# Performance work log

Measured on AMD Instinct MI355X. Metric: run time of the kernel, lower is better.

The kernel has to match this reference:

```python
import jax, jax.numpy as jnp
import numpy as np

N = 50000       # nodes
E = 500000      # edges
F_IN = 64       # input feature dim
F_OUT = 64      # hidden/output dim
K = 3           # diffusion filter order
C = F_IN + F_OUT  # concat dim seen by each DConv


def _xavier(k, shape):
    fan_in, fan_out = shape[-2], shape[-1]
    lim = float(np.sqrt(6.0 / (fan_in + fan_out)))
    return jax.random.uniform(k, shape, jnp.float32, -lim, lim)


def setup_inputs() -> dict:
    key = jax.random.key(0)
    ks = jax.random.split(key, 8)
    X = jax.random.normal(ks[0], (N, F_IN), jnp.float32)
    H = jax.random.normal(ks[1], (N, F_OUT), jnp.float32)
    # ring edges guarantee every node has in-degree >= 1 and out-degree >= 1
    base = jnp.arange(N, dtype=jnp.int32)
    row = jnp.concatenate([base, jax.random.randint(ks[2], (E - N,), 0, N, jnp.int32)])
    col = jnp.concatenate([jnp.roll(base, 1), jax.random.randint(ks[3], (E - N,), 0, N, jnp.int32)])
    edge_index = jnp.stack([row, col])  # [2, E]
    W_z = _xavier(ks[4], (2, K, C, F_OUT))
    W_r = _xavier(ks[5], (2, K, C, F_OUT))
    W_h = _xavier(ks[6], (2, K, C, F_OUT))
    b = jnp.zeros((F_OUT,), jnp.float32)
    return {"X": X, "edge_index": edge_index, "H": H,
            "W_z": W_z, "b_z": b, "W_r": W_r, "b_r": b, "W_h": W_h, "b_h": b}


def _dconv(Xc, row, col, norm_out, norm_in, W, b):
    # PyG propagate: gather source (row) features, scale by edge norm, scatter-add to target (col)
    def prop(x, norm):
        return jax.ops.segment_sum(norm[:, None] * x[row], col, num_segments=N)
    Tx_0 = Xc
    Hout = Xc @ (W[0, 0] + W[1, 0])
    Tx_1_o = prop(Xc, norm_out)
    Tx_1_i = prop(Xc, norm_in)
    Hout = Hout + Tx_1_o @ W[0, 1] + Tx_1_i @ W[1, 1]
    for k in range(2, K):
        Tx_2_o = 2.0 * prop(Tx_1_o, norm_out) - Tx_0
        Tx_2_i = 2.0 * prop(Tx_1_i, norm_in) - Tx_0
        Hout = Hout + Tx_2_o @ W[0, k] + Tx_2_i @ W[1, k]
        # faithful to original: Tx_1 is never reassigned, so Tx_0 stays Xc
        Tx_0, Tx_1_o, Tx_1_i = Xc, Tx_2_o, Tx_2_i
    return Hout + b


def reference(X, edge_index, H, W_z, b_z, W_r, b_r, W_h, b_h):
    row, col = edge_index[0], edge_index[1]
    deg_out = jnp.zeros((N,), jnp.float32).at[row].add(1.0)
    deg_in = jnp.zeros((N,), jnp.float32).at[col].add(1.0)
    norm_out = (1.0 / deg_out)[row]
    norm_in = (1.0 / deg_in)[row]
    XH = jnp.concatenate([X, H], axis=1)
    Z = jax.nn.sigmoid(_dconv(XH, row, col, norm_out, norm_in, W_z, b_z))
    R = jax.nn.sigmoid(_dconv(XH, row, col, norm_out, norm_in, W_r, b_r))
    XHR = jnp.concatenate([X, H * R], axis=1)
    H_tilde = jnp.tanh(_dconv(XHR, row, col, norm_out, norm_in, W_h, b_h))
    H_new = Z * H + (1.0 - Z) * H_tilde
    # NaN infill with mean of non-NaN entries (faithful to original)
    mask = jnp.isnan(H_new)
    H_new = jnp.where(mask, jnp.nanmean(H_new), H_new)
    return H_new
```

## Files before the change

kernel.cpp:

```cpp
#include <hip/hip_runtime.h>
#include <hip/hip_bf16.h>
#include <math.h>

#define N_NODES 50000
#define N_EDGES 500000
#define C_DIM 128

typedef __attribute__((ext_vector_type(8))) short bf8;
typedef __attribute__((ext_vector_type(4))) float f32x4;

__device__ __forceinline__ float bflo(unsigned u) { return __uint_as_float(u << 16); }
__device__ __forceinline__ float bfhi(unsigned u) { return __uint_as_float(u & 0xffff0000u); }
__device__ __forceinline__ unsigned short f2bfu(float f) {
    __hip_bfloat16 h = __float2bfloat16(f);
    unsigned short u;
    __builtin_memcpy(&u, &h, 2);
    return u;
}
__device__ __forceinline__ unsigned packbf(float a, float b) {
    return ((unsigned)f2bfu(b) << 16) | f2bfu(a);
}


__global__ void count_deg(const int* __restrict__ row, const int* __restrict__ col,
                          int* __restrict__ dout, int* __restrict__ din, int e) {
    int i = blockIdx.x * blockDim.x + threadIdx.x;
    if (i >= e) return;
    atomicAdd(&dout[row[i]], 1);
    atomicAdd(&din[col[i]], 1);
}

__global__ void scan_block(const int* __restrict__ counts, int* __restrict__ excl,
                           int* __restrict__ blocksums, int n) {
    __shared__ int tmp[1024];
    int tid = threadIdx.x;
    int gid = blockIdx.x * 1024 + tid;
    int v = (gid < n) ? counts[gid] : 0;
    tmp[tid] = v;
    __syncthreads();
    for (int off = 1; off < 1024; off <<= 1) {
        int t = (tid >= off) ? tmp[tid - off] : 0;
        __syncthreads();
        tmp[tid] += t;
        __syncthreads();
    }
    int incl = tmp[tid];
    if (gid < n) excl[gid] = incl - v;
    if (tid == 1023) blocksums[blockIdx.x] = incl;
}

__global__ void scan_sums(int* __restrict__ blocksums, int nb) {
    __shared__ int tmp[64];
    int tid = threadIdx.x;
    int v = (tid < nb) ? blocksums[tid] : 0;
    tmp[tid] = v;
    __syncthreads();
    for (int off = 1; off < 64; off <<= 1) {
        int t = (tid >= off) ? tmp[tid - off] : 0;
        __syncthreads();
        tmp[tid] += t;
        __syncthreads();
    }
    if (tid < nb) blocksums[tid] = tmp[tid] - v;
}

__global__ void scan_add(int* __restrict__ rowptr, const int* __restrict__ blocksums,
                         int* __restrict__ cursor, const int* __restrict__ dout,
                         const int* __restrict__ din, float2* __restrict__ winv,
                         int n, int e_total) {
    int gid = blockIdx.x * blockDim.x + threadIdx.x;
    if (gid < n) {
        int v = rowptr[gid] + blocksums[gid >> 10];
        rowptr[gid] = v;
        cursor[gid] = v;
        winv[gid] = make_float2(1.0f / (float)dout[gid], 1.0f / (float)din[gid]);
    }
    if (gid == n) rowptr[n] = e_total;
}

__global__ void build_csr(const int* __restrict__ row, const int* __restrict__ col,
                          const float2* __restrict__ winv,
                          int* __restrict__ cursor, int* __restrict__ src,
                          float2* __restrict__ w, int e) {
    int i = blockIdx.x * blockDim.x + threadIdx.x;
    if (i >= e) return;
    int r = row[i], c = col[i];
    int pos = atomicAdd(&cursor[c], 1);
    src[pos] = r;
    w[pos] = winv[r];
}

__device__ __forceinline__ float wraw(const float* W, int d, int kk, int k, int j) {
    return W[((d * 3 + kk) * 128 + k) * 64 + j];
}

__global__ void pack_weights(const float* __restrict__ Wz, const float* __restrict__ Wr,
                             const float* __restrict__ Wh,
                             unsigned short* __restrict__ Wzr_t,
                             unsigned short* __restrict__ Wh_t) {
    int i = blockIdx.x * blockDim.x + threadIdx.x;
    if (i < 128 * 640) {
        int k = i % 640;
        int nn = i / 640;
        const float* W = (nn < 64) ? Wz : Wr;
        int j = nn & 63;
        float v;
        if (k < 128) {
            v = wraw(W, 0, 0, k, j) + wraw(W, 1, 0, k, j);
        } else {
            int k2 = k - 128;
            int kk = (k2 >= 256) ? 2 : 1;
            int k3 = k2 & 255;
            int p = k3 >> 2, sub = k3 & 3;
            v = wraw(W, sub >> 1, kk, 2 * p + (sub & 1), j);
        }
        Wzr_t[i] = f2bfu(v);
    } else if (i < 128 * 640 + 64 * 640) {
        int i2 = i - 128 * 640;
        int k = i2 % 640;
        int j = i2 / 640;
        float v;
        if (k < 64) {
            v = wraw(Wh, 0, 0, k, j) + wraw(Wh, 1, 0, k, j);
        } else if (k < 320) {
            int k2 = k - 64;
            int kk = (k2 >= 128) ? 2 : 1;
            int k3 = k2 & 127;
            int p = k3 >> 2, sub = k3 & 3;
            v = wraw(Wh, sub >> 1, kk, 2 * p + (sub & 1), j);
        } else if (k < 384) {
            int rr = k - 320;
            v = wraw(Wh, 0, 0, 64 + rr, j) + wraw(Wh, 1, 0, 64 + rr, j);
        } else {
            int k2 = k - 384;
            int kk = (k2 >= 128) ? 2 : 1;
            int k3 = k2 & 127;
            int p = k3 >> 2, sub = k3 & 3;
            v = wraw(Wh, sub >> 1, kk, 64 + 2 * p + (sub & 1), j);
        }
        Wh_t[i2] = f2bfu(v);
    }
}


__global__ void concat_xh(const float* __restrict__ X, const float* __restrict__ H,
                          unsigned short* __restrict__ XH, int n) {
    int i = blockIdx.x * blockDim.x + threadIdx.x;
    if (i >= n * C_DIM) return;
    int r = i >> 7, c = i & 127;
    float v = (c < 64) ? X[r * 64 + c] : H[r * 64 + (c - 64)];
    XH[i] = f2bfu(v);
}


__global__ void prop1_128(const unsigned short* __restrict__ S,
                          const int* __restrict__ rowptr, const int* __restrict__ src,
                          const float2* __restrict__ w,
                          unsigned short* __restrict__ P1, int n) {
    int node = (blockIdx.x * blockDim.x + threadIdx.x) >> 6;
    int lane = threadIdx.x & 63;
    if (node >= n) return;
    int beg = rowptr[node], end = rowptr[node + 1];
    float ao0 = 0.f, ao1 = 0.f, ai0 = 0.f, ai1 = 0.f;
    int j = beg;
    for (; j + 4 <= end; j += 4) {
        int s0 = src[j], s1 = src[j + 1], s2 = src[j + 2], s3 = src[j + 3];
        float2 w0 = w[j], w1 = w[j + 1], w2 = w[j + 2], w3 = w[j + 3];
        unsigned u0 = *(const unsigned*)(S + (size_t)s0 * 128 + 2 * lane);
        unsigned u1 = *(const unsigned*)(S + (size_t)s1 * 128 + 2 * lane);
        unsigned u2 = *(const unsigned*)(S + (size_t)s2 * 128 + 2 * lane);
        unsigned u3 = *(const unsigned*)(S + (size_t)s3 * 128 + 2 * lane);
        ao0 = fmaf(w0.x, bflo(u0), ao0); ao1 = fmaf(w0.x, bfhi(u0), ao1);
        ai0 = fmaf(w0.y, bflo(u0), ai0); ai1 = fmaf(w0.y, bfhi(u0), ai1);
        ao0 = fmaf(w1.x, bflo(u1), ao0); ao1 = fmaf(w1.x, bfhi(u1), ao1);
        ai0 = fmaf(w1.y, bflo(u1), ai0); ai1 = fmaf(w1.y, bfhi(u1), ai1);
        ao0 = fmaf(w2.x, bflo(u2), ao0); ao1 = fmaf(w2.x, bfhi(u2), ao1);
        ai0 = fmaf(w2.y, bflo(u2), ai0); ai1 = fmaf(w2.y, bfhi(u2), ai1);
        ao0 = fmaf(w3.x, bflo(u3), ao0); ao1 = fmaf(w3.x, bfhi(u3), ao1);
        ai0 = fmaf(w3.y, bflo(u3), ai0); ai1 = fmaf(w3.y, bfhi(u3), ai1);
    }
    for (; j < end; ++j) {
        int s = src[j];
        float2 wv = w[j];
        unsigned u = *(const unsigned*)(S + (size_t)s * 128 + 2 * lane);
        ao0 = fmaf(wv.x, bflo(u), ao0); ao1 = fmaf(wv.x, bfhi(u), ao1);
        ai0 = fmaf(wv.y, bflo(u), ai0); ai1 = fmaf(wv.y, bfhi(u), ai1);
    }
    uint2 out;
    out.x = packbf(ao0, ao1);
    out.y = packbf(ai0, ai1);
    *(uint2*)(P1 + (size_t)node * 256 + 4 * lane) = out;
}

__global__ void prop2_128(const unsigned short* __restrict__ P1,
                          const unsigned short* __restrict__ Xc,
                          const int* __restrict__ rowptr, const int* __restrict__ src,
                          const float2* __restrict__ w,
                          unsigned short* __restrict__ P2, int n) {
    int node = (blockIdx.x * blockDim.x + threadIdx.x) >> 6;
    int lane = threadIdx.x & 63;
    if (node >= n) return;
    int beg = rowptr[node], end = rowptr[node + 1];
    float ao0 = 0.f, ao1 = 0.f, ai0 = 0.f, ai1 = 0.f;
    int j = beg;
    for (; j + 4 <= end; j += 4) {
        int s0 = src[j], s1 = src[j + 1], s2 = src[j + 2], s3 = src[j + 3];
        float2 w0 = w[j], w1 = w[j + 1], w2 = w[j + 2], w3 = w[j + 3];
        uint2 v0 = *(const uint2*)(P1 + (size_t)s0 * 256 + 4 * lane);
        uint2 v1 = *(const uint2*)(P1 + (size_t)s1 * 256 + 4 * lane);
        uint2 v2 = *(const uint2*)(P1 + (size_t)s2 * 256 + 4 * lane);
        uint2 v3 = *(const uint2*)(P1 + (size_t)s3 * 256 + 4 * lane);
        ao0 = fmaf(w0.x, bflo(v0.x), ao0); ao1 = fmaf(w0.x, bfhi(v0.x), ao1);
        ai0 = fmaf(w0.y, bflo(v0.y), ai0); ai1 = fmaf(w0.y, bfhi(v0.y), ai1);
        ao0 = fmaf(w1.x, bflo(v1.x), ao0); ao1 = fmaf(w1.x, bfhi(v1.x), ao1);
        ai0 = fmaf(w1.y, bflo(v1.y), ai0); ai1 = fmaf(w1.y, bfhi(v1.y), ai1);
        ao0 = fmaf(w2.x, bflo(v2.x), ao0); ao1 = fmaf(w2.x, bfhi(v2.x), ao1);
        ai0 = fmaf(w2.y, bflo(v2.y), ai0); ai1 = fmaf(w2.y, bfhi(v2.y), ai1);
        ao0 = fmaf(w3.x, bflo(v3.x), ao0); ao1 = fmaf(w3.x, bfhi(v3.x), ao1);
        ai0 = fmaf(w3.y, bflo(v3.y), ai0); ai1 = fmaf(w3.y, bfhi(v3.y), ai1);
    }
    for (; j < end; ++j) {
        int s = src[j];
        float2 wv = w[j];
        uint2 v = *(const uint2*)(P1 + (size_t)s * 256 + 4 * lane);
        ao0 = fmaf(wv.x, bflo(v.x), ao0); ao1 = fmaf(wv.x, bfhi(v.x), ao1);
        ai0 = fmaf(wv.y, bflo(v.y), ai0); ai1 = fmaf(wv.y, bfhi(v.y), ai1);
    }
    unsigned ux = *(const unsigned*)(Xc + (size_t)node * 128 + 2 * lane);
    float x0 = bflo(ux), x1 = bfhi(ux);
    uint2 out;
    out.x = packbf(2.f * ao0 - x0, 2.f * ao1 - x1);
    out.y = packbf(2.f * ai0 - x0, 2.f * ai1 - x1);
    *(uint2*)(P2 + (size_t)node * 256 + 4 * lane) = out;
}

__global__ void prop1_64(const unsigned short* __restrict__ HR,
                         const int* __restrict__ rowptr, const int* __restrict__ src,
                         const float2* __restrict__ w,
                         unsigned short* __restrict__ Q1, int n) {
    int tid = blockIdx.x * blockDim.x + threadIdx.x;
    int lane = tid & 63;
    int node = (tid >> 6) * 2 + (lane >> 5);
    int p = lane & 31;
    if (node >= n) return;
    int beg = rowptr[node], end = rowptr[node + 1];
    float ao0 = 0.f, ao1 = 0.f, ai0 = 0.f, ai1 = 0.f;
    int j = beg;
    for (; j + 4 <= end; j += 4) {
        int s0 = src[j], s1 = src[j + 1], s2 = src[j + 2], s3 = src[j + 3];
        float2 w0 = w[j], w1 = w[j + 1], w2 = w[j + 2], w3 = w[j + 3];
        unsigned u0 = *(const unsigned*)(HR + (size_t)s0 * 64 + 2 * p);
        unsigned u1 = *(const unsigned*)(HR + (size_t)s1 * 64 + 2 * p);
        unsigned u2 = *(const unsigned*)(HR + (size_t)s2 * 64 + 2 * p);
        unsigned u3 = *(const unsigned*)(HR + (size_t)s3 * 64 + 2 * p);
        ao0 = fmaf(w0.x, bflo(u0), ao0); ao1 = fmaf(w0.x, bfhi(u0), ao1);
        ai0 = fmaf(w0.y, bflo(u0), ai0); ai1 = fmaf(w0.y, bfhi(u0), ai1);
        ao0 = fmaf(w1.x, bflo(u1), ao0); ao1 = fmaf(w1.x, bfhi(u1), ao1);
        ai0 = fmaf(w1.y, bflo(u1), ai0); ai1 = fmaf(w1.y, bfhi(u1), ai1);
        ao0 = fmaf(w2.x, bflo(u2), ao0); ao1 = fmaf(w2.x, bfhi(u2), ao1);
        ai0 = fmaf(w2.y, bflo(u2), ai0); ai1 = fmaf(w2.y, bfhi(u2), ai1);
        ao0 = fmaf(w3.x, bflo(u3), ao0); ao1 = fmaf(w3.x, bfhi(u3), ao1);
        ai0 = fmaf(w3.y, bflo(u3), ai0); ai1 = fmaf(w3.y, bfhi(u3), ai1);
    }
    for (; j < end; ++j) {
        int s = src[j];
        float2 wv = w[j];
        unsigned u = *(const unsigned*)(HR + (size_t)s * 64 + 2 * p);
        ao0 = fmaf(wv.x, bflo(u), ao0); ao1 = fmaf(wv.x, bfhi(u), ao1);
        ai0 = fmaf(wv.y, bflo(u), ai0); ai1 = fmaf(wv.y, bfhi(u), ai1);
    }
    uint2 out;
    out.x = packbf(ao0, ao1);
    out.y = packbf(ai0, ai1);
    *(uint2*)(Q1 + (size_t)node * 128 + 4 * p) = out;
}

__global__ void prop2_64(const unsigned short* __restrict__ Q1,
                         const unsigned short* __restrict__ HR,
                         const int* __restrict__ rowptr, const int* __restrict__ src,
                         const float2* __restrict__ w,
                         unsigned short* __restrict__ Q2, int n) {
    int tid = blockIdx.x * blockDim.x + threadIdx.x;
    int lane = tid & 63;
    int node = (tid >> 6) * 2 + (lane >> 5);
    int p = lane & 31;
    if (node >= n) return;
    int beg = rowptr[node], end = rowptr[node + 1];
    float ao0 = 0.f, ao1 = 0.f, ai0 = 0.f, ai1 = 0.f;
    int j = beg;
    for (; j + 4 <= end; j += 4) {
        int s0 = src[j], s1 = src[j + 1], s2 = src[j + 2], s3 = src[j + 3];
        float2 w0 = w[j], w1 = w[j + 1], w2 = w[j + 2], w3 = w[j + 3];
        uint2 v0 = *(const uint2*)(Q1 + (size_t)s0 * 128 + 4 * p);
        uint2 v1 = *(const uint2*)(Q1 + (size_t)s1 * 128 + 4 * p);
        uint2 v2 = *(const uint2*)(Q1 + (size_t)s2 * 128 + 4 * p);
        uint2 v3 = *(const uint2*)(Q1 + (size_t)s3 * 128 + 4 * p);
        ao0 = fmaf(w0.x, bflo(v0.x), ao0); ao1 = fmaf(w0.x, bfhi(v0.x), ao1);
        ai0 = fmaf(w0.y, bflo(v0.y), ai0); ai1 = fmaf(w0.y, bfhi(v0.y), ai1);
        ao0 = fmaf(w1.x, bflo(v1.x), ao0); ao1 = fmaf(w1.x, bfhi(v1.x), ao1);
        ai0 = fmaf(w1.y, bflo(v1.y), ai0); ai1 = fmaf(w1.y, bfhi(v1.y), ai1);
        ao0 = fmaf(w2.x, bflo(v2.x), ao0); ao1 = fmaf(w2.x, bfhi(v2.x), ao1);
        ai0 = fmaf(w2.y, bflo(v2.y), ai0); ai1 = fmaf(w2.y, bfhi(v2.y), ai1);
        ao0 = fmaf(w3.x, bflo(v3.x), ao0); ao1 = fmaf(w3.x, bfhi(v3.x), ao1);
        ai0 = fmaf(w3.y, bflo(v3.y), ai0); ai1 = fmaf(w3.y, bfhi(v3.y), ai1);
    }
    for (; j < end; ++j) {
        int s = src[j];
        float2 wv = w[j];
        uint2 v = *(const uint2*)(Q1 + (size_t)s * 128 + 4 * p);
        ao0 = fmaf(wv.x, bflo(v.x), ao0); ao1 = fmaf(wv.x, bfhi(v.x), ao1);
        ai0 = fmaf(wv.y, bflo(v.y), ai0); ai1 = fmaf(wv.y, bfhi(v.y), ai1);
    }
    unsigned ux = *(const unsigned*)(HR + (size_t)node * 64 + 2 * p);
    float x0 = bflo(ux), x1 = bfhi(ux);
    uint2 out;
    out.x = packbf(2.f * ao0 - x0, 2.f * ao1 - x1);
    out.y = packbf(2.f * ai0 - x0, 2.f * ai1 - x1);
    *(uint2*)(Q2 + (size_t)node * 128 + 4 * p) = out;
}


__global__ __launch_bounds__(256) void gemm_zr_mfma(
    const unsigned short* __restrict__ XH, const unsigned short* __restrict__ P1,
    const unsigned short* __restrict__ P2,
    const unsigned short* __restrict__ Wt, const float* __restrict__ bz,
    const float* __restrict__ br, const float* __restrict__ H,
    float* __restrict__ Zf, unsigned short* __restrict__ HR, int n) {
    int lane = threadIdx.x & 63;
    int wave = blockIdx.x * 4 + (threadIdx.x >> 6);
    int rowbase = wave * 32;
    if (rowbase >= n) return;
    int lr = lane & 15;
    int quad = lane >> 4;
    int r0 = rowbase + lr;       if (r0 >= n) r0 = n - 1;
    int r1 = rowbase + 16 + lr;  if (r1 >= n) r1 = n - 1;

    f32x4 zero = {0.f, 0.f, 0.f, 0.f};
    f32x4 acc[2][8];
#pragma unroll
    for (int a = 0; a < 2; ++a)
#pragma unroll
        for (int b = 0; b < 8; ++b) acc[a][b] = zero;

    const unsigned short* bases[3] = {XH, P1, P2};
    const int strides[3] = {128, 256, 256};
    const int nch[3] = {4, 8, 8};
    int kg = 0;
#pragma unroll
    for (int sg = 0; sg < 3; ++sg) {
        const unsigned short* A0 = bases[sg] + (size_t)r0 * strides[sg] + quad * 8;
        const unsigned short* A1 = bases[sg] + (size_t)r1 * strides[sg] + quad * 8;
#pragma unroll
        for (int kk = 0; kk < nch[sg]; ++kk) {
            bf8 a0 = *(const bf8*)(A0 + kk * 32);
            bf8 a1 = *(const bf8*)(A1 + kk * 32);
#pragma unroll
            for (int nt = 0; nt < 8; ++nt) {
                bf8 b = *(const bf8*)(Wt + (size_t)(nt * 16 + lr) * 640 + kg + kk * 32 + quad * 8);
                acc[0][nt] = __builtin_amdgcn_mfma_f32_16x16x32_bf16(a0, b, acc[0][nt], 0, 0, 0);
                acc[1][nt] = __builtin_amdgcn_mfma_f32_16x16x32_bf16(a1, b, acc[1][nt], 0, 0, 0);
            }
        }
        kg += nch[sg] * 32;
    }
#pragma unroll
    for (int mt = 0; mt < 2; ++mt)
#pragma unroll
        for (int reg = 0; reg < 4; ++reg) {
            int r = rowbase + mt * 16 + quad * 4 + reg;
            if (r >= n) continue;
#pragma unroll
            for (int nt = 0; nt < 8; ++nt) {
                int c = nt * 16 + lr;
                float bias = (c < 64) ? bz[c] : br[c - 64];
                float v = acc[mt][nt][reg] + bias;
                float s = 1.f / (1.f + expf(-v));
                if (nt < 4) {
                    Zf[(size_t)r * 64 + c] = s;
                } else {
                    int c2 = c - 64;
                    HR[(size_t)r * 64 + c2] = f2bfu(H[(size_t)r * 64 + c2] * s);
                }
            }
        }
}

__global__ __launch_bounds__(256) void gemm_h_mfma(
    const unsigned short* __restrict__ XH, const unsigned short* __restrict__ P1,
    const unsigned short* __restrict__ P2, const unsigned short* __restrict__ HR,
    const unsigned short* __restrict__ Q1, const unsigned short* __restrict__ Q2,
    const unsigned short* __restrict__ Wt, const float* __restrict__ bh,
    const float* __restrict__ Zf, const float* __restrict__ H,
    float* __restrict__ out, int n) {
    int lane = threadIdx.x & 63;
    int wave = blockIdx.x * 4 + (threadIdx.x >> 6);
    int rowbase = wave * 32;
    if (rowbase >= n) return;
    int lr = lane & 15;
    int quad = lane >> 4;
    int r0 = rowbase + lr;       if (r0 >= n) r0 = n - 1;
    int r1 = rowbase + 16 + lr;  if (r1 >= n) r1 = n - 1;

    f32x4 zero = {0.f, 0.f, 0.f, 0.f};
    f32x4 acc[2][4];
#pragma unroll
    for (int a = 0; a < 2; ++a)
#pragma unroll
        for (int b = 0; b < 4; ++b) acc[a][b] = zero;

    const unsigned short* bases[6] = {XH, P1, P2, HR, Q1, Q2};
    const int strides[6] = {128, 256, 256, 64, 128, 128};
    const int nch[6] = {2, 4, 4, 2, 4, 4};
    int kg = 0;
#pragma unroll
    for (int sg = 0; sg < 6; ++sg) {
        const unsigned short* A0 = bases[sg] + (size_t)r0 * strides[sg] + quad * 8;
        const unsigned short* A1 = bases[sg] + (size_t)r1 * strides[sg] + quad * 8;
#pragma unroll
        for (int kk = 0; kk < nch[sg]; ++kk) {
            bf8 a0 = *(const bf8*)(A0 + kk * 32);
            bf8 a1 = *(const bf8*)(A1 + kk * 32);
#pragma unroll
            for (int nt = 0; nt < 4; ++nt) {
                bf8 b = *(const bf8*)(Wt + (size_t)(nt * 16 + lr) * 640 + kg + kk * 32 + quad * 8);
                acc[0][nt] = __builtin_amdgcn_mfma_f32_16x16x32_bf16(a0, b, acc[0][nt], 0, 0, 0);
                acc[1][nt] = __builtin_amdgcn_mfma_f32_16x16x32_bf16(a1, b, acc[1][nt], 0, 0, 0);
            }
        }
        kg += nch[sg] * 32;
    }
#pragma unroll
    for (int mt = 0; mt < 2; ++mt)
#pragma unroll
        for (int reg = 0; reg < 4; ++reg) {
            int r = rowbase + mt * 16 + quad * 4 + reg;
            if (r >= n) continue;
#pragma unroll
            for (int nt = 0; nt < 4; ++nt) {
                int c = nt * 16 + lr;
                float ht = tanhf(acc[mt][nt][reg] + bh[c]);
                float z = Zf[(size_t)r * 64 + c];
                float h_old = H[(size_t)r * 64 + c];
                out[(size_t)r * 64 + c] = z * h_old + (1.f - z) * ht;
            }
        }
}


static inline size_t rup(size_t x) { return (x + 63) & ~(size_t)63; }

extern "C" void kernel_launch(void* const* d_in, const int* in_sizes, int n_in,
                              void* d_out, int out_size, void* d_ws, size_t ws_size,
                              hipStream_t stream) {
    const float* X  = (const float*)d_in[0];
    const int*   EI = (const int*)d_in[1];
    const float* H  = (const float*)d_in[2];
    const float* Wz = (const float*)d_in[3];
    const float* bz = (const float*)d_in[4];
    const float* Wr = (const float*)d_in[5];
    const float* br = (const float*)d_in[6];
    const float* Wh = (const float*)d_in[7];
    const float* bh = (const float*)d_in[8];
    float* out = (float*)d_out;

    const int* row = EI;
    const int* col = EI + N_EDGES;

    char* ws = (char*)d_ws;
    size_t off = 0;
    auto carve = [&](size_t bytes) { void* p = ws + off; off += rup(bytes); return p; };

    int*   deg_out   = (int*)carve(N_NODES * 4);
    int*   deg_in    = (int*)carve(N_NODES * 4);
    int*   rowptr    = (int*)carve((N_NODES + 1) * 4);
    int*   cursor    = (int*)carve(N_NODES * 4);
    int*   blocksums = (int*)carve(64 * 4);
    float2* winv     = (float2*)carve(N_NODES * 8);
    int*   csr_src   = (int*)carve(N_EDGES * 4);
    float2* csr_w    = (float2*)carve(N_EDGES * 8);
    unsigned short* XH = (unsigned short*)carve((size_t)N_NODES * 128 * 2);
    unsigned short* P1 = (unsigned short*)carve((size_t)N_NODES * 256 * 2);
    unsigned short* P2 = (unsigned short*)carve((size_t)N_NODES * 256 * 2);
    unsigned short* HR = (unsigned short*)carve((size_t)N_NODES * 64 * 2);
    unsigned short* Q1 = (unsigned short*)carve((size_t)N_NODES * 128 * 2);
    unsigned short* Q2 = (unsigned short*)carve((size_t)N_NODES * 128 * 2);
    float* Zf          = (float*)carve((size_t)N_NODES * 64 * 4);
    unsigned short* Wzr_t = (unsigned short*)carve(128 * 640 * 2);
    unsigned short* Wh_t  = (unsigned short*)carve(64 * 640 * 2);

    hipMemsetAsync(deg_out, 0, rup(N_NODES * 4) + rup(N_NODES * 4), stream);
    count_deg<<<(N_EDGES + 255) / 256, 256, 0, stream>>>(row, col, deg_out, deg_in, N_EDGES);

    int nblk = (N_NODES + 1023) / 1024;
    scan_block<<<nblk, 1024, 0, stream>>>(deg_in, rowptr, blocksums, N_NODES);
    scan_sums<<<1, 64, 0, stream>>>(blocksums, nblk);
    scan_add<<<(N_NODES + 1 + 255) / 256, 256, 0, stream>>>(rowptr, blocksums, cursor,
                                                            deg_out, deg_in, winv, N_NODES, N_EDGES);

    build_csr<<<(N_EDGES + 255) / 256, 256, 0, stream>>>(row, col, winv, cursor,
                                                         csr_src, csr_w, N_EDGES);

    pack_weights<<<(128 * 640 + 64 * 640 + 255) / 256, 256, 0, stream>>>(Wz, Wr, Wh, Wzr_t, Wh_t);

    concat_xh<<<(N_NODES * C_DIM + 255) / 256, 256, 0, stream>>>(X, H, XH, N_NODES);

    int blocks128 = (N_NODES * 64 + 255) / 256;
    prop1_128<<<blocks128, 256, 0, stream>>>(XH, rowptr, csr_src, csr_w, P1, N_NODES);
    prop2_128<<<blocks128, 256, 0, stream>>>(P1, XH, rowptr, csr_src, csr_w, P2, N_NODES);

    int gemm_blocks = (N_NODES + 127) / 128;
    gemm_zr_mfma<<<gemm_blocks, 256, 0, stream>>>(XH, P1, P2, Wzr_t, bz, br, H, Zf, HR, N_NODES);

    int blocks64 = ((N_NODES + 1) / 2 * 64 + 255) / 256;
    prop1_64<<<blocks64, 256, 0, stream>>>(HR, rowptr, csr_src, csr_w, Q1, N_NODES);
    prop2_64<<<blocks64, 256, 0, stream>>>(Q1, HR, rowptr, csr_src, csr_w, Q2, N_NODES);

    gemm_h_mfma<<<gemm_blocks, 256, 0, stream>>>(XH, P1, P2, HR, Q1, Q2,
                                                 Wh_t, bh, Zf, H, out, N_NODES);
}
```

Measured before the change: 400.4 us.

## Widen per-lane gather loads in propagation and stage GEMM weights in LDS

The four SpMM propagation kernels now give each lane 4 (or 8) bf16 features instead of 2 (or 4), packing two or four nodes per wavefront. This raises the bytes per gather load and the number of rows in flight per wave. Both MFMA GEMMs now stage weight chunks in shared memory with a padded stride and split each block's 64 rows by 2 M-halves and 2 N-halves across its four waves. The intent is to cut redundant global weight reads, at the cost of barriers per K chunk and a smaller tile per wave.

```diff
diff --git a/kernel.cpp b/kernel.cpp
--- a/kernel.cpp
+++ b/kernel.cpp
@@ -157,39 +157,36 @@
                           const int* __restrict__ rowptr, const int* __restrict__ src,
                           const float2* __restrict__ w,
                           unsigned short* __restrict__ P1, int n) {
-    int node = (blockIdx.x * blockDim.x + threadIdx.x) >> 6;
-    int lane = threadIdx.x & 63;
+    int tid = blockIdx.x * blockDim.x + threadIdx.x;
+    int lane = tid & 63;
+    int node = ((tid >> 6) << 1) + (lane >> 5);
+    int p = lane & 31;
     if (node >= n) return;
     int beg = rowptr[node], end = rowptr[node + 1];
-    float ao0 = 0.f, ao1 = 0.f, ai0 = 0.f, ai1 = 0.f;
+    float ao0 = 0.f, ao1 = 0.f, ao2 = 0.f, ao3 = 0.f;
+    float ai0 = 0.f, ai1 = 0.f, ai2 = 0.f, ai3 = 0.f;
     int j = beg;
+#define P1STEP(s_, w_) {                                                     \
+        uint2 u = *(const uint2*)(S + (size_t)(s_) * 128 + 4 * p);           \
+        float c0 = bflo(u.x), c1 = bfhi(u.x), c2 = bflo(u.y), c3 = bfhi(u.y);\
+        ao0 = fmaf(w_.x, c0, ao0); ao1 = fmaf(w_.x, c1, ao1);                \
+        ao2 = fmaf(w_.x, c2, ao2); ao3 = fmaf(w_.x, c3, ao3);                \
+        ai0 = fmaf(w_.y, c0, ai0); ai1 = fmaf(w_.y, c1, ai1);                \
+        ai2 = fmaf(w_.y, c2, ai2); ai3 = fmaf(w_.y, c3, ai3); }
     for (; j + 4 <= end; j += 4) {
         int s0 = src[j], s1 = src[j + 1], s2 = src[j + 2], s3 = src[j + 3];
         float2 w0 = w[j], w1 = w[j + 1], w2 = w[j + 2], w3 = w[j + 3];
-        unsigned u0 = *(const unsigned*)(S + (size_t)s0 * 128 + 2 * lane);
-        unsigned u1 = *(const unsigned*)(S + (size_t)s1 * 128 + 2 * lane);
-        unsigned u2 = *(const unsigned*)(S + (size_t)s2 * 128 + 2 * lane);
-        unsigned u3 = *(const unsigned*)(S + (size_t)s3 * 128 + 2 * lane);
-        ao0 = fmaf(w0.x, bflo(u0), ao0); ao1 = fmaf(w0.x, bfhi(u0), ao1);
-        ai0 = fmaf(w0.y, bflo(u0), ai0); ai1 = fmaf(w0.y, bfhi(u0), ai1);
-        ao0 = fmaf(w1.x, bflo(u1), ao0); ao1 = fmaf(w1.x, bfhi(u1), ao1);
-        ai0 = fmaf(w1.y, bflo(u1), ai0); ai1 = fmaf(w1.y, bfhi(u1), ai1);
-        ao0 = fmaf(w2.x, bflo(u2), ao0); ao1 = fmaf(w2.x, bfhi(u2), ao1);
-        ai0 = fmaf(w2.y, bflo(u2), ai0); ai1 = fmaf(w2.y, bfhi(u2), ai1);
-        ao0 = fmaf(w3.x, bflo(u3), ao0); ao1 = fmaf(w3.x, bfhi(u3), ao1);
-        ai0 = fmaf(w3.y, bflo(u3), ai0); ai1 = fmaf(w3.y, bfhi(u3), ai1);
+        P1STEP(s0, w0); P1STEP(s1, w1); P1STEP(s2, w2); P1STEP(s3, w3);
     }
     for (; j < end; ++j) {
-        int s = src[j];
-        float2 wv = w[j];
-        unsigned u = *(const unsigned*)(S + (size_t)s * 128 + 2 * lane);
-        ao0 = fmaf(wv.x, bflo(u), ao0); ao1 = fmaf(wv.x, bfhi(u), ao1);
-        ai0 = fmaf(wv.y, bflo(u), ai0); ai1 = fmaf(wv.y, bfhi(u), ai1);
-    }
-    uint2 out;
-    out.x = packbf(ao0, ao1);
-    out.y = packbf(ai0, ai1);
-    *(uint2*)(P1 + (size_t)node * 256 + 4 * lane) = out;
+        int s = src[j]; float2 wv = w[j];
+        P1STEP(s, wv);
+    }
+#undef P1STEP
+    uint4 o;
+    o.x = packbf(ao0, ao1); o.y = packbf(ai0, ai1);
+    o.z = packbf(ao2, ao3); o.w = packbf(ai2, ai3);
+    *(uint4*)(P1 + (size_t)node * 256 + 8 * p) = o;
 }
 
 __global__ void prop2_128(const unsigned short* __restrict__ P1,
@@ -197,41 +194,39 @@
                           const int* __restrict__ rowptr, const int* __restrict__ src,
                           const float2* __restrict__ w,
                           unsigned short* __restrict__ P2, int n) {
-    int node = (blockIdx.x * blockDim.x + threadIdx.x) >> 6;
-    int lane = threadIdx.x & 63;
+    int tid = blockIdx.x * blockDim.x + threadIdx.x;
+    int lane = tid & 63;
+    int node = ((tid >> 6) << 1) + (lane >> 5);
+    int p = lane & 31;
     if (node >= n) return;
     int beg = rowptr[node], end = rowptr[node + 1];
-    float ao0 = 0.f, ao1 = 0.f, ai0 = 0.f, ai1 = 0.f;
+    float oa = 0.f, ob = 0.f, oc = 0.f, od = 0.f;
+    float ia = 0.f, ib = 0.f, ic = 0.f, id = 0.f;
     int j = beg;
+#define P2STEP(s_, w_) {                                                     \
+        uint4 v = *(const uint4*)(P1 + (size_t)(s_) * 256 + 8 * p);          \
+        oa = fmaf(w_.x, bflo(v.x), oa); ob = fmaf(w_.x, bfhi(v.x), ob);      \
+        ia = fmaf(w_.y, bflo(v.y), ia); ib = fmaf(w_.y, bfhi(v.y), ib);      \
+        oc = fmaf(w_.x, bflo(v.z), oc); od = fmaf(w_.x, bfhi(v.z), od);      \
+        ic = fmaf(w_.y, bflo(v.w), ic); id = fmaf(w_.y, bfhi(v.w), id); }
     for (; j + 4 <= end; j += 4) {
         int s0 = src[j], s1 = src[j + 1], s2 = src[j + 2], s3 = src[j + 3];
         float2 w0 = w[j], w1 = w[j + 1], w2 = w[j + 2], w3 = w[j + 3];
-        uint2 v0 = *(const uint2*)(P1 + (size_t)s0 * 256 + 4 * lane);
-        uint2 v1 = *(const uint2*)(P1 + (size_t)s1 * 256 + 4 * lane);
-        uint2 v2 = *(const uint2*)(P1 + (size_t)s2 * 256 + 4 * lane);
-        uint2 v3 = *(const uint2*)(P1 + (size_t)s3 * 256 + 4 * lane);
-        ao0 = fmaf(w0.x, bflo(v0.x), ao0); ao1 = fmaf(w0.x, bfhi(v0.x), ao1);
-        ai0 = fmaf(w0.y, bflo(v0.y), ai0); ai1 = fmaf(w0.y, bfhi(v0.y), ai1);
-        ao0 = fmaf(w1.x, bflo(v1.x), ao0); ao1 = fmaf(w1.x, bfhi(v1.x), ao1);
-        ai0 = fmaf(w1.y, bflo(v1.y), ai0); ai1 = fmaf(w1.y, bfhi(v1.y), ai1);
-        ao0 = fmaf(w2.x, bflo(v2.x), ao0); ao1 = fmaf(w2.x, bfhi(v2.x), ao1);
-        ai0 = fmaf(w2.y, bflo(v2.y), ai0); ai1 = fmaf(w2.y, bfhi(v2.y), ai1);
-        ao0 = fmaf(w3.x, bflo(v3.x), ao0); ao1 = fmaf(w3.x, bfhi(v3.x), ao1);
-        ai0 = fmaf(w3.y, bflo(v3.y), ai0); ai1 = fmaf(w3.y, bfhi(v3.y), ai1);
+        P2STEP(s0, w0); P2STEP(s1, w1); P2STEP(s2, w2); P2STEP(s3, w3);
     }
     for (; j < end; ++j) {
-        int s = src[j];
-        float2 wv = w[j];
-        uint2 v = *(const uint2*)(P1 + (size_t)s * 256 + 4 * lane);
-        ao0 = fmaf(wv.x, bflo(v.x), ao0); ao1 = fmaf(wv.x, bfhi(v.x), ao1);
-        ai0 = fmaf(wv.y, bflo(v.y), ai0); ai1 = fmaf(wv.y, bfhi(v.y), ai1);
-    }
-    unsigned ux = *(const unsigned*)(Xc + (size_t)node * 128 + 2 * lane);
-    float x0 = bflo(ux), x1 = bfhi(ux);
-    uint2 out;
-    out.x = packbf(2.f * ao0 - x0, 2.f * ao1 - x1);
-    out.y = packbf(2.f * ai0 - x0, 2.f * ai1 - x1);
-    *(uint2*)(P2 + (size_t)node * 256 + 4 * lane) = out;
+        int s = src[j]; float2 wv = w[j];
+        P2STEP(s, wv);
+    }
+#undef P2STEP
+    uint2 ux = *(const uint2*)(Xc + (size_t)node * 128 + 4 * p);
+    float xa = bflo(ux.x), xb = bfhi(ux.x), xc = bflo(ux.y), xd = bfhi(ux.y);
+    uint4 o;
+    o.x = packbf(2.f * oa - xa, 2.f * ob - xb);
+    o.y = packbf(2.f * ia - xa, 2.f * ib - xb);
+    o.z = packbf(2.f * oc - xc, 2.f * od - xd);
+    o.w = packbf(2.f * ic - xc, 2.f * id - xd);
+    *(uint4*)(P2 + (size_t)node * 256 + 8 * p) = o;
 }
 
 __global__ void prop1_64(const unsigned short* __restrict__ HR,
@@ -240,39 +235,34 @@
                          unsigned short* __restrict__ Q1, int n) {
     int tid = blockIdx.x * blockDim.x + threadIdx.x;
     int lane = tid & 63;
-    int node = (tid >> 6) * 2 + (lane >> 5);
-    int p = lane & 31;
+    int node = ((tid >> 6) << 2) + (lane >> 4);
+    int p = lane & 15;
     if (node >= n) return;
     int beg = rowptr[node], end = rowptr[node + 1];
-    float ao0 = 0.f, ao1 = 0.f, ai0 = 0.f, ai1 = 0.f;
+    float ao0 = 0.f, ao1 = 0.f, ao2 = 0.f, ao3 = 0.f;
+    float ai0 = 0.f, ai1 = 0.f, ai2 = 0.f, ai3 = 0.f;
     int j = beg;
+#define Q1STEP(s_, w_) {                                                     \
+        uint2 u = *(const uint2*)(HR + (size_t)(s_) * 64 + 4 * p);           \
+        float c0 = bflo(u.x), c1 = bfhi(u.x), c2 = bflo(u.y), c3 = bfhi(u.y);\
+        ao0 = fmaf(w_.x, c0, ao0); ao1 = fmaf(w_.x, c1, ao1);                \
+        ao2 = fmaf(w_.x, c2, ao2); ao3 = fmaf(w_.x, c3, ao3);                \
+        ai0 = fmaf(w_.y, c0, ai0); ai1 = fmaf(w_.y, c1, ai1);                \
+        ai2 = fmaf(w_.y, c2, ai2); ai3 = fmaf(w_.y, c3, ai3); }
     for (; j + 4 <= end; j += 4) {
         int s0 = src[j], s1 = src[j + 1], s2 = src[j + 2], s3 = src[j + 3];
         float2 w0 = w[j], w1 = w[j + 1], w2 = w[j + 2], w3 = w[j + 3];
-        unsigned u0 = *(const unsigned*)(HR + (size_t)s0 * 64 + 2 * p);
-        unsigned u1 = *(const unsigned*)(HR + (size_t)s1 * 64 + 2 * p);
-        unsigned u2 = *(const unsigned*)(HR + (size_t)s2 * 64 + 2 * p);
-        unsigned u3 = *(const unsigned*)(HR + (size_t)s3 * 64 + 2 * p);
-        ao0 = fmaf(w0.x, bflo(u0), ao0); ao1 = fmaf(w0.x, bfhi(u0), ao1);
-        ai0 = fmaf(w0.y, bflo(u0), ai0); ai1 = fmaf(w0.y, bfhi(u0), ai1);
-        ao0 = fmaf(w1.x, bflo(u1), ao0); ao1 = fmaf(w1.x, bfhi(u1), ao1);
-        ai0 = fmaf(w1.y, bflo(u1), ai0); ai1 = fmaf(w1.y, bfhi(u1), ai1);
-        ao0 = fmaf(w2.x, bflo(u2), ao0); ao1 = fmaf(w2.x, bfhi(u2), ao1);
-        ai0 = fmaf(w2.y, bflo(u2), ai0); ai1 = fmaf(w2.y, bfhi(u2), ai1);
-        ao0 = fmaf(w3.x, bflo(u3), ao0); ao1 = fmaf(w3.x, bfhi(u3), ao1);
-        ai0 = fmaf(w3.y, bflo(u3), ai0); ai1 = fmaf(w3.y, bfhi(u3), ai1);
+        Q1STEP(s0, w0); Q1STEP(s1, w1); Q1STEP(s2, w2); Q1STEP(s3, w3);
     }
     for (; j < end; ++j) {
-        int s = src[j];
-        float2 wv = w[j];
-        unsigned u = *(const unsigned*)(HR + (size_t)s * 64 + 2 * p);
-        ao0 = fmaf(wv.x, bflo(u), ao0); ao1 = fmaf(wv.x, bfhi(u), ao1);
-        ai0 = fmaf(wv.y, bflo(u), ai0); ai1 = fmaf(wv.y, bfhi(u), ai1);
-    }
-    uint2 out;
-    out.x = packbf(ao0, ao1);
-    out.y = packbf(ai0, ai1);
-    *(uint2*)(Q1 + (size_t)node * 128 + 4 * p) = out;
+        int s = src[j]; float2 wv = w[j];
+        Q1STEP(s, wv);
+    }
+#undef Q1STEP
+    uint4 o;
+    o.x = packbf(ao0, ao1); o.y = packbf(ai0, ai1);
+    o.z = packbf(ao2, ao3); o.w = packbf(ai2, ai3);
+    *(uint4*)(Q1 + (size_t)node * 128 + 8 * p) = o;
 }
 
 __global__ void prop2_64(const unsigned short* __restrict__ Q1,
@@ -282,41 +272,37 @@
                          unsigned short* __restrict__ Q2, int n) {
     int tid = blockIdx.x * blockDim.x + threadIdx.x;
     int lane = tid & 63;
-    int node = (tid >> 6) * 2 + (lane >> 5);
-    int p = lane & 31;
+    int node = ((tid >> 6) << 2) + (lane >> 4);
+    int p = lane & 15;
     if (node >= n) return;
     int beg = rowptr[node], end = rowptr[node + 1];
-    float ao0 = 0.f, ao1 = 0.f, ai0 = 0.f, ai1 = 0.f;
+    float oa = 0.f, ob = 0.f, oc = 0.f, od = 0.f;
+    float ia = 0.f, ib = 0.f, ic = 0.f, id = 0.f;
     int j = beg;
+#define Q2STEP(s_, w_) {                                                     \
+        uint4 v = *(const uint4*)(Q1 + (size_t)(s_) * 128 + 8 * p);          \
+        oa = fmaf(w_.x, bflo(v.x), oa); ob = fmaf(w_.x, bfhi(v.x), ob);      \
+        ia = fmaf(w_.y, bflo(v.y), ia); ib = fmaf(w_.y, bfhi(v.y), ib);      \
+        oc = fmaf(w_.x, bflo(v.z), oc); od = fmaf(w_.x, bfhi(v.z), od);      \
+        ic = fmaf(w_.y, bflo(v.w), ic); id = fmaf(w_.y, bfhi(v.w), id); }
     for (; j + 4 <= end; j += 4) {
         int s0 = src[j], s1 = src[j + 1], s2 = src[j + 2], s3 = src[j + 3];
         float2 w0 = w[j], w1 = w[j + 1], w2 = w[j + 2], w3 = w[j + 3];
-        uint2 v0 = *(const uint2*)(Q1 + (size_t)s0 * 128 + 4 * p);
-        uint2 v1 = *(const uint2*)(Q1 + (size_t)s1 * 128 + 4 * p);
-        uint2 v2 = *(const uint2*)(Q1 + (size_t)s2 * 128 + 4 * p);
-        uint2 v3 = *(const uint2*)(Q1 + (size_t)s3 * 128 + 4 * p);
-        ao0 = fmaf(w0.x, bflo(v0.x), ao0); ao1 = fmaf(w0.x, bfhi(v0.x), ao1);
-        ai0 = fmaf(w0.y, bflo(v0.y), ai0); ai1 = fmaf(w0.y, bfhi(v0.y), ai1);
-        ao0 = fmaf(w1.x, bflo(v1.x), ao0); ao1 = fmaf(w1.x, bfhi(v1.x), ao1);
-        ai0 = fmaf(w1.y, bflo(v1.y), ai0); ai1 = fmaf(w1.y, bfhi(v1.y), ai1);
-        ao0 = fmaf(w2.x, bflo(v2.x), ao0); ao1 = fmaf(w2.x, bfhi(v2.x), ao1);
-        ai0 = fmaf(w2.y, bflo(v2.y), ai0); ai1 = fmaf(w2.y, bfhi(v2.y), ai1);
-        ao0 = fmaf(w3.x, bflo(v3.x), ao0); ao1 = fmaf(w3.x, bfhi(v3.x), ao1);
-        ai0 = fmaf(w3.y, bflo(v3.y), ai0); ai1 = fmaf(w3.y, bfhi(v3.y), ai1);
+        Q2STEP(s0, w0); Q2STEP(s1, w1); Q2STEP(s2, w2); Q2STEP(s3, w3);
     }
     for (; j < end; ++j) {
-        int s = src[j];
-        float2 wv = w[j];
-        uint2 v = *(const uint2*)(Q1 + (size_t)s * 128 + 4 * p);
-        ao0 = fmaf(wv.x, bflo(v.x), ao0); ao1 = fmaf(wv.x, bfhi(v.x), ao1);
-        ai0 = fmaf(wv.y, bflo(v.y), ai0); ai1 = fmaf(wv.y, bfhi(v.y), ai1);
-    }
-    unsigned ux = *(const unsigned*)(HR + (size_t)node * 64 + 2 * p);
-    float x0 = bflo(ux), x1 = bfhi(ux);
-    uint2 out;
-    out.x = packbf(2.f * ao0 - x0, 2.f * ao1 - x1);
-    out.y = packbf(2.f * ai0 - x0, 2.f * ai1 - x1);
-    *(uint2*)(Q2 + (size_t)node * 128 + 4 * p) = out;
+        int s = src[j]; float2 wv = w[j];
+        Q2STEP(s, wv);
+    }
+#undef Q2STEP
+    uint2 ux = *(const uint2*)(HR + (size_t)node * 64 + 4 * p);
+    float xa = bflo(ux.x), xb = bfhi(ux.x), xc = bflo(ux.y), xd = bfhi(ux.y);
+    uint4 o;
+    o.x = packbf(2.f * oa - xa, 2.f * ob - xb);
+    o.y = packbf(2.f * ia - xa, 2.f * ib - xb);
+    o.z = packbf(2.f * oc - xc, 2.f * od - xd);
+    o.w = packbf(2.f * ic - xc, 2.f * id - xd);
+    *(uint4*)(Q2 + (size_t)node * 128 + 8 * p) = o;
 }
 
 
@@ -326,42 +312,53 @@
     const unsigned short* __restrict__ Wt, const float* __restrict__ bz,
     const float* __restrict__ br, const float* __restrict__ H,
     float* __restrict__ Zf, unsigned short* __restrict__ HR, int n) {
-    int lane = threadIdx.x & 63;
-    int wave = blockIdx.x * 4 + (threadIdx.x >> 6);
-    int rowbase = wave * 32;
-    if (rowbase >= n) return;
-    int lr = lane & 15;
-    int quad = lane >> 4;
+    __shared__ uint2 Wl[128 * 66];
+    int tid = threadIdx.x;
+    int lane = tid & 63;
+    int wid = tid >> 6;
+    int mhalf = wid & 1, nhalf = wid >> 1;
+    int rowbase = blockIdx.x * 64 + mhalf * 32;
+    int lr = lane & 15, quad = lane >> 4;
     int r0 = rowbase + lr;       if (r0 >= n) r0 = n - 1;
     int r1 = rowbase + 16 + lr;  if (r1 >= n) r1 = n - 1;
 
     f32x4 zero = {0.f, 0.f, 0.f, 0.f};
-    f32x4 acc[2][8];
+    f32x4 acc[2][4];
 #pragma unroll
     for (int a = 0; a < 2; ++a)
 #pragma unroll
-        for (int b = 0; b < 8; ++b) acc[a][b] = zero;
-
-    const unsigned short* bases[3] = {XH, P1, P2};
-    const int strides[3] = {128, 256, 256};
-    const int nch[3] = {4, 8, 8};
-    int kg = 0;
-#pragma unroll
-    for (int sg = 0; sg < 3; ++sg) {
-        const unsigned short* A0 = bases[sg] + (size_t)r0 * strides[sg] + quad * 8;
-        const unsigned short* A1 = bases[sg] + (size_t)r1 * strides[sg] + quad * 8;
-#pragma unroll
-        for (int kk = 0; kk < nch[sg]; ++kk) {
+        for (int b = 0; b < 4; ++b) acc[a][b] = zero;
+
+    const unsigned short* Ab[5] = {XH, P1, P1, P2, P2};
+    const int Astr[5] = {128, 256, 256, 256, 256};
+    const int Aoff[5] = {0, 0, 128, 0, 128};
+
+    for (int c = 0; c < 5; ++c) {
+        const unsigned short* Wsrc = Wt + c * 128;
+        for (int i = tid; i < 128 * 16; i += 256) {
+            int nrow = i >> 4, kp = i & 15;
+            uint4 v = *(const uint4*)(Wsrc + (size_t)nrow * 640 + kp * 8);
+            *(uint4*)&Wl[nrow * 66 + kp * 2] = v;
+        }
+        __syncthreads();
+        const unsigned short* A0 = Ab[c] + (size_t)r0 * Astr[c] + Aoff[c] + quad * 8;
+        const unsigned short* A1 = Ab[c] + (size_t)r1 * Astr[c] + Aoff[c] + quad * 8;
+#pragma unroll
+        for (int kk = 0; kk < 4; ++kk) {
             bf8 a0 = *(const bf8*)(A0 + kk * 32);
             bf8 a1 = *(const bf8*)(A1 + kk * 32);
 #pragma unroll
-            for (int nt = 0; nt < 8; ++nt) {
-                bf8 b = *(const bf8*)(Wt + (size_t)(nt * 16 + lr) * 640 + kg + kk * 32 + quad * 8);
-                acc[0][nt] = __builtin_amdgcn_mfma_f32_16x16x32_bf16(a0, b, acc[0][nt], 0, 0, 0);
-                acc[1][nt] = __builtin_amdgcn_mfma_f32_16x16x32_bf16(a1, b, acc[1][nt], 0, 0, 0);
+            for (int nt = 0; nt < 4; ++nt) {
+                int nrow = nhalf * 64 + nt * 16 + lr;
+                int base = nrow * 66 + kk * 8 + quad * 2;
+                union { bf8 v; uint2 h[2]; } bb;
+                bb.h[0] = Wl[base];
+                bb.h[1] = Wl[base + 1];
+                acc[0][nt] = __builtin_amdgcn_mfma_f32_16x16x32_bf16(a0, bb.v, acc[0][nt], 0, 0, 0);
+                acc[1][nt] = __builtin_amdgcn_mfma_f32_16x16x32_bf16(a1, bb.v, acc[1][nt], 0, 0, 0);
             }
         }
-        kg += nch[sg] * 32;
+        __syncthreads();
     }
 #pragma unroll
     for (int mt = 0; mt < 2; ++mt)
@@ -370,15 +367,15 @@
             int r = rowbase + mt * 16 + quad * 4 + reg;
             if (r >= n) continue;
 #pragma unroll
-            for (int nt = 0; nt < 8; ++nt) {
-                int c = nt * 16 + lr;
-                float bias = (c < 64) ? bz[c] : br[c - 64];
+            for (int nt = 0; nt < 4; ++nt) {
+                int cidx = nhalf * 64 + nt * 16 + lr;
+                float bias = (cidx < 64) ? bz[cidx] : br[cidx - 64];
                 float v = acc[mt][nt][reg] + bias;
                 float s = 1.f / (1.f + expf(-v));
-                if (nt < 4) {
-                    Zf[(size_t)r * 64 + c] = s;
+                if (cidx < 64) {
+                    Zf[(size_t)r * 64 + cidx] = s;
                 } else {
-                    int c2 = c - 64;
+                    int c2 = cidx - 64;
                     HR[(size_t)r * 64 + c2] = f2bfu(H[(size_t)r * 64 + c2] * s);
                 }
             }
@@ -392,42 +389,57 @@
     const unsigned short* __restrict__ Wt, const float* __restrict__ bh,
     const float* __restrict__ Zf, const float* __restrict__ H,
     float* __restrict__ out, int n) {
-    int lane = threadIdx.x & 63;
-    int wave = blockIdx.x * 4 + (threadIdx.x >> 6);
-    int rowbase = wave * 32;
-    if (rowbase >= n) return;
-    int lr = lane & 15;
-    int quad = lane >> 4;
+    __shared__ uint2 Wl[64 * 66];
+    int tid = threadIdx.x;
+    int lane = tid & 63;
+    int wid = tid >> 6;
+    int mhalf = wid & 1, nhalf = wid >> 1;
+    int rowbase = blockIdx.x * 64 + mhalf * 32;
+    int lr = lane & 15, quad = lane >> 4;
     int r0 = rowbase + lr;       if (r0 >= n) r0 = n - 1;
     int r1 = rowbase + 16 + lr;  if (r1 >= n) r1 = n - 1;
 
     f32x4 zero = {0.f, 0.f, 0.f, 0.f};
-    f32x4 acc[2][4];
+    f32x4 acc[2][2];
 #pragma unroll
     for (int a = 0; a < 2; ++a)
 #pragma unroll
-        for (int b = 0; b < 4; ++b) acc[a][b] = zero;
-
-    const unsigned short* bases[6] = {XH, P1, P2, HR, Q1, Q2};
-    const int strides[6] = {128, 256, 256, 64, 128, 128};
-    const int nch[6] = {2, 4, 4, 2, 4, 4};
-    int kg = 0;
-#pragma unroll
+        for (int b = 0; b < 2; ++b) acc[a][b] = zero;
+
+    const unsigned short* Ab[6] = {XH, P1, P2, HR, Q1, Q2};
+    const int Astr[6] = {128, 256, 256, 64, 128, 128};
+    const int Aklen[6] = {64, 128, 128, 64, 128, 128};
+    const int Akg[6] = {0, 64, 192, 320, 384, 512};
+
     for (int sg = 0; sg < 6; ++sg) {
-        const unsigned short* A0 = bases[sg] + (size_t)r0 * strides[sg] + quad * 8;
-        const unsigned short* A1 = bases[sg] + (size_t)r1 * strides[sg] + quad * 8;
-#pragma unroll
-        for (int kk = 0; kk < nch[sg]; ++kk) {
+        int klen = Aklen[sg];
+        int units = 64 * (klen >> 3);
+        const unsigned short* Wsrc = Wt + Akg[sg];
+        for (int i = tid; i < units; i += 256) {
+            int kcnt = klen >> 3;
+            int nrow = i / kcnt, kp = i % kcnt;
+            uint4 v = *(const uint4*)(Wsrc + (size_t)nrow * 640 + kp * 8);
+            *(uint4*)&Wl[nrow * 66 + kp * 2] = v;
+        }
+        __syncthreads();
+        const unsigned short* A0 = Ab[sg] + (size_t)r0 * Astr[sg] + quad * 8;
+        const unsigned short* A1 = Ab[sg] + (size_t)r1 * Astr[sg] + quad * 8;
+        int nkk = klen >> 5;
+        for (int kk = 0; kk < nkk; ++kk) {
             bf8 a0 = *(const bf8*)(A0 + kk * 32);
             bf8 a1 = *(const bf8*)(A1 + kk * 32);
 #pragma unroll
-            for (int nt = 0; nt < 4; ++nt) {
-                bf8 b = *(const bf8*)(Wt + (size_t)(nt * 16 + lr) * 640 + kg + kk * 32 + quad * 8);
-                acc[0][nt] = __builtin_amdgcn_mfma_f32_16x16x32_bf16(a0, b, acc[0][nt], 0, 0, 0);
-                acc[1][nt] = __builtin_amdgcn_mfma_f32_16x16x32_bf16(a1, b, acc[1][nt], 0, 0, 0);
+            for (int nt = 0; nt < 2; ++nt) {
+                int nrow = nhalf * 32 + nt * 16 + lr;
+                int base = nrow * 66 + kk * 8 + quad * 2;
+                union { bf8 v; uint2 h[2]; } bb;
+                bb.h[0] = Wl[base];
+                bb.h[1] = Wl[base + 1];
+                acc[0][nt] = __builtin_amdgcn_mfma_f32_16x16x32_bf16(a0, bb.v, acc[0][nt], 0, 0, 0);
+                acc[1][nt] = __builtin_amdgcn_mfma_f32_16x16x32_bf16(a1, bb.v, acc[1][nt], 0, 0, 0);
             }
         }
-        kg += nch[sg] * 32;
+        __syncthreads();
     }
 #pragma unroll
     for (int mt = 0; mt < 2; ++mt)
@@ -436,12 +448,12 @@
             int r = rowbase + mt * 16 + quad * 4 + reg;
             if (r >= n) continue;
 #pragma unroll
-            for (int nt = 0; nt < 4; ++nt) {
-                int c = nt * 16 + lr;
-                float ht = tanhf(acc[mt][nt][reg] + bh[c]);
-                float z = Zf[(size_t)r * 64 + c];
-                float h_old = H[(size_t)r * 64 + c];
-                out[(size_t)r * 64 + c] = z * h_old + (1.f - z) * ht;
+            for (int nt = 0; nt < 2; ++nt) {
+                int cidx = nhalf * 32 + nt * 16 + lr;
+                float ht = tanhf(acc[mt][nt][reg] + bh[cidx]);
+                float z = Zf[(size_t)r * 64 + cidx];
+                float h_old = H[(size_t)r * 64 + cidx];
+                out[(size_t)r * 64 + cidx] = z * h_old + (1.f - z) * ht;
             }
         }
 }
@@ -504,16 +516,16 @@
 
     concat_xh<<<(N_NODES * C_DIM + 255) / 256, 256, 0, stream>>>(X, H, XH, N_NODES);
 
-    int blocks128 = (N_NODES * 64 + 255) / 256;
-    prop1_128<<<blocks128, 256, 0, stream>>>(XH, rowptr, csr_src, csr_w, P1, N_NODES);
-    prop2_128<<<blocks128, 256, 0, stream>>>(P1, XH, rowptr, csr_src, csr_w, P2, N_NODES);
-
-    int gemm_blocks = (N_NODES + 127) / 128;
+    int blocks_p128 = (((N_NODES + 1) / 2) * 64 + 255) / 256;
+    prop1_128<<<blocks_p128, 256, 0, stream>>>(XH, rowptr, csr_src, csr_w, P1, N_NODES);
+    prop2_128<<<blocks_p128, 256, 0, stream>>>(P1, XH, rowptr, csr_src, csr_w, P2, N_NODES);
+
+    int gemm_blocks = (N_NODES + 63) / 64;
     gemm_zr_mfma<<<gemm_blocks, 256, 0, stream>>>(XH, P1, P2, Wzr_t, bz, br, H, Zf, HR, N_NODES);
 
-    int blocks64 = ((N_NODES + 1) / 2 * 64 + 255) / 256;
-    prop1_64<<<blocks64, 256, 0, stream>>>(HR, rowptr, csr_src, csr_w, Q1, N_NODES);
-    prop2_64<<<blocks64, 256, 0, stream>>>(Q1, HR, rowptr, csr_src, csr_w, Q2, N_NODES);
+    int blocks_p64 = (((N_NODES + 3) / 4) * 64 + 255) / 256;
+    prop1_64<<<blocks_p64, 256, 0, stream>>>(HR, rowptr, csr_src, csr_w, Q1, N_NODES);
+    prop2_64<<<blocks_p64, 256, 0, stream>>>(Q1, HR, rowptr, csr_src, csr_w, Q2, N_NODES);
 
     gemm_h_mfma<<<gemm_blocks, 256, 0, stream>>>(XH, P1, P2, HR, Q1, Q2,
                                                  Wh_t, bh, Zf, H, out, N_NODES);
```

Measured after the change: 393.0 us. No clear change (-1.9%).
